# Performance work log

Hardware: AMD Instinct MI355X
Metric: run time of the kernel (lower is better)

Reference implementation:

```python
import jax, jax.numpy as jnp
import numpy as np

B, S, T = 64, 64, 64          # batch, encoder seq len, decoder context_length
V, D, H, L = 32000, 512, 1024, 256  # vocab, embed, hidden, latent


def _gru_cell(x, h, W_ih, W_hh, b_ih, b_hh):
    # PyTorch GRUCell math. x:[B,D_in], h:[B,H]
    gi = x @ W_ih.T + b_ih            # [B,3H]
    gh = h @ W_hh.T + b_hh            # [B,3H]
    i_r, i_z, i_n = jnp.split(gi, 3, axis=-1)
    h_r, h_z, h_n = jnp.split(gh, 3, axis=-1)
    r = jax.nn.sigmoid(i_r + h_r)
    z = jax.nn.sigmoid(i_z + h_z)
    n = jnp.tanh(i_n + r * h_n)
    return (1.0 - z) * n + z * h


def setup_inputs() -> dict:
    key = jax.random.key(0)
    ks = jax.random.split(key, 16)
    s = 0.02
    inp = {
        "x": jax.random.randint(ks[0], (B, S), 0, V),
        "eps": jax.random.normal(ks[1], (B, L), dtype=jnp.float32),
        "E": jax.random.normal(ks[2], (V, D), dtype=jnp.float32) * s,
        # encoder GRU
        "W_ih_enc": jax.random.normal(ks[3], (3 * H, D), dtype=jnp.float32) * s,
        "W_hh_enc": jax.random.normal(ks[4], (3 * H, H), dtype=jnp.float32) * s,
        "b_ih_enc": jnp.zeros((3 * H,), jnp.float32),
        "b_hh_enc": jnp.zeros((3 * H,), jnp.float32),
        # latent heads
        "W_mu": jax.random.normal(ks[5], (L, H), dtype=jnp.float32) * s,
        "b_mu": jnp.zeros((L,), jnp.float32),
        "W_lv": jax.random.normal(ks[6], (L, H), dtype=jnp.float32) * s,
        "b_lv": jnp.zeros((L,), jnp.float32),
        # decoder proj_h: latent -> hidden
        "W_proj": jax.random.normal(ks[7], (H, L), dtype=jnp.float32) * s,
        "b_proj": jnp.zeros((H,), jnp.float32),
        # decoder GRU cell
        "W_ih_dec": jax.random.normal(ks[8], (3 * H, D), dtype=jnp.float32) * s,
        "W_hh_dec": jax.random.normal(ks[9], (3 * H, H), dtype=jnp.float32) * s,
        "b_ih_dec": jnp.zeros((3 * H,), jnp.float32),
        "b_hh_dec": jnp.zeros((3 * H,), jnp.float32),
        # output projection hidden -> vocab
        "W_out": jax.random.normal(ks[10], (V, H), dtype=jnp.float32) * s,
        "b_out": jnp.zeros((V,), jnp.float32),
    }
    return inp


def reference(x, eps, E, W_ih_enc, W_hh_enc, b_ih_enc, b_hh_enc,
              W_mu, b_mu, W_lv, b_lv, W_proj, b_proj,
              W_ih_dec, W_hh_dec, b_ih_dec, b_hh_dec, W_out, b_out):
    # --- encode ---
    xe = E[x]                                  # [B,S,D]
    h0 = jnp.zeros((x.shape[0], H), xe.dtype)

    def enc_step(h, xt):
        h = _gru_cell(xt, h, W_ih_enc, W_hh_enc, b_ih_enc, b_hh_enc)
        return h, None

    h_last, _ = jax.lax.scan(enc_step, h0, jnp.swapaxes(xe, 0, 1))  # scan over S
    mu = h_last @ W_mu.T + b_mu                # [B,L]
    logvar = h_last @ W_lv.T + b_lv            # [B,L]

    # --- reparametrize ---
    z = mu + eps * jnp.exp(0.5 * logvar)       # [B,L]

    h_dec0 = z @ W_proj.T + b_proj             # [B,H]
    x0 = jnp.zeros((x.shape[0], D), xe.dtype)  # step 0 input is None -> zeros

    def dec_step(carry, _):
        h, xin = carry
        h = _gru_cell(xin, h, W_ih_dec, W_hh_dec, b_ih_dec, b_hh_dec)
        logits = h @ W_out.T + b_out           # [B,V]
        nxt = jnp.argmax(logits, axis=-1)      # [B]
        return (h, E[nxt]), logits

    _, logits_seq = jax.lax.scan(dec_step, (h_dec0, x0), None, length=T)
    outputs = jnp.swapaxes(logits_seq, 0, 1)   # [B,T,V]
    return outputs, mu, logvar
```

## Files before the change

kernel.cpp:

```cpp
#include <hip/hip_runtime.h>

#define B_ 64
#define S_ 64
#define T_ 64
#define V_ 32000
#define D_ 512
#define H_ 1024
#define L_ 256

typedef _Float16 f16;
typedef __attribute__((ext_vector_type(4))) _Float16 f16x4;
typedef __attribute__((ext_vector_type(8))) _Float16 f16x8;
typedef __attribute__((ext_vector_type(16))) float f32x16;

#define INV2048 (1.0f / 2048.0f)

__device__ __forceinline__ void write_frag(f16* __restrict__ Aohi, f16* __restrict__ Aolo,
                                           int b, int j, float hv) {
  const f16 hi = (f16)hv;
  const f16 lo = (f16)((hv - (float)hi) * 2048.0f);
  const long long fo =
      (((long long)(b >> 5) * 64 + (j >> 4)) * 64 + ((b & 31) + 32 * ((j >> 3) & 1))) * 8 + (j & 7);
  Aohi[fo] = hi;
  Aolo[fo] = lo;
}

template <int K>
__global__ __launch_bounds__(256) void k_pack_wf(
    const float* __restrict__ W, f16* __restrict__ Bhi, f16* __restrict__ Blo)
{
  const int n = blockIdx.x;
  const int k = threadIdx.x * 4;
  if (k >= K) return;
  float4 w = *reinterpret_cast<const float4*>(W + (long long)n * K + k);
  float wv[4] = {w.x, w.y, w.z, w.w};
  f16x4 hi, lo;
#pragma unroll
  for (int i = 0; i < 4; ++i) {
    const f16 h = (f16)wv[i];
    hi[i] = h;
    lo[i] = (f16)((wv[i] - (float)h) * 2048.0f);
  }
  const int nt = n >> 5;
  const int lane = (n & 31) + 32 * ((k >> 3) & 1);
  const int ks = k >> 4;
  const long long off = (((long long)nt * (K / 16) + ks) * 64 + lane) * 8 + (k & 7);
  *reinterpret_cast<f16x4*>(Bhi + off) = hi;
  *reinterpret_cast<f16x4*>(Blo + off) = lo;
}

__global__ __launch_bounds__(128) void k_pack_xe(
    const int* __restrict__ x, const float* __restrict__ E,
    f16* __restrict__ XAhi, f16* __restrict__ XAlo)
{
  const int m = blockIdx.x;
  const int s = m >> 6, b = m & 63;
  const int k = threadIdx.x * 4;
  const long long tok = x[b * S_ + s];
  float4 w = *reinterpret_cast<const float4*>(E + tok * D_ + k);
  float wv[4] = {w.x, w.y, w.z, w.w};
  f16x4 hi, lo;
#pragma unroll
  for (int i = 0; i < 4; ++i) {
    const f16 h = (f16)wv[i];
    hi[i] = h;
    lo[i] = (f16)((wv[i] - (float)h) * 2048.0f);
  }
  const int mt = m >> 5;
  const int lane = (m & 31) + 32 * ((k >> 3) & 1);
  const int ks = k >> 4;
  const long long off = (((long long)mt * 32 + ks) * 64 + lane) * 8 + (k & 7);
  *reinterpret_cast<f16x4*>(XAhi + off) = hi;
  *reinterpret_cast<f16x4*>(XAlo + off) = lo;
}

__global__ __launch_bounds__(256) void k_gates_mfma(
    const f16* __restrict__ XAhi, const f16* __restrict__ XAlo,
    const f16* __restrict__ Bhi, const f16* __restrict__ Blo,
    const float* __restrict__ b_ih, float* __restrict__ Gi)
{
  __shared__ float cand[4][64][33];
  const int tid = threadIdx.x;
  const int lane = tid & 63;
  const int wv = __builtin_amdgcn_readfirstlane(tid >> 6);
  const int s = blockIdx.x / 24;
  const int ng = blockIdx.x % 24;
  const int nt = ng * 4 + wv;

  f32x16 aM0, aM1, aLa0, aLa1, aLb0, aLb1;
#pragma unroll
  for (int i = 0; i < 16; ++i) {
    aM0[i] = 0.f; aM1[i] = 0.f; aLa0[i] = 0.f; aLa1[i] = 0.f; aLb0[i] = 0.f; aLb1[i] = 0.f;
  }

  const f16x8* pB_h = reinterpret_cast<const f16x8*>(Bhi) + ((long long)nt * 32) * 64 + lane;
  const f16x8* pB_l = reinterpret_cast<const f16x8*>(Blo) + ((long long)nt * 32) * 64 + lane;
  const f16x8* pA_h = reinterpret_cast<const f16x8*>(XAhi) + ((long long)s * 64) * 64 + lane;
  const f16x8* pA_l = reinterpret_cast<const f16x8*>(XAlo) + ((long long)s * 64) * 64 + lane;

#pragma unroll 4
  for (int ks = 0; ks < 32; ++ks) {
    const int o = ks * 64;
    f16x8 bh = pB_h[o];
    f16x8 bl = pB_l[o];
    f16x8 a0 = pA_h[o];
    f16x8 a1 = pA_h[o + 32 * 64];
    f16x8 l0 = pA_l[o];
    f16x8 l1 = pA_l[o + 32 * 64];
    aM0 = __builtin_amdgcn_mfma_f32_32x32x16_f16(a0, bh, aM0, 0, 0, 0);
    aM1 = __builtin_amdgcn_mfma_f32_32x32x16_f16(a1, bh, aM1, 0, 0, 0);
    aLa0 = __builtin_amdgcn_mfma_f32_32x32x16_f16(a0, bl, aLa0, 0, 0, 0);
    aLa1 = __builtin_amdgcn_mfma_f32_32x32x16_f16(a1, bl, aLa1, 0, 0, 0);
    aLb0 = __builtin_amdgcn_mfma_f32_32x32x16_f16(l0, bh, aLb0, 0, 0, 0);
    aLb1 = __builtin_amdgcn_mfma_f32_32x32x16_f16(l1, bh, aLb1, 0, 0, 0);
  }

  {
    const int l = lane & 31;
    const int rbase = 4 * (lane >> 5);
#pragma unroll
    for (int reg = 0; reg < 16; ++reg) {
      const int row = (reg & 3) + 8 * (reg >> 2) + rbase;
      cand[wv][row][l] = aM0[reg] + (aLa0[reg] + aLb0[reg]) * INV2048;
      cand[wv][row + 32][l] = aM1[reg] + (aLa1[reg] + aLb1[reg]) * INV2048;
    }
  }
  __syncthreads();
  const int bn0 = ng * 128;
#pragma unroll
  for (int i = 0; i < 8; ++i) {
    const int idx = i * 256 + tid;
    const int b4 = (idx & 15) * 4;
    const int nl = idx >> 4;
    const float bi = b_ih[bn0 + nl];
    float4 o;
    o.x = cand[nl >> 5][b4 + 0][nl & 31] + bi;
    o.y = cand[nl >> 5][b4 + 1][nl & 31] + bi;
    o.z = cand[nl >> 5][b4 + 2][nl & 31] + bi;
    o.w = cand[nl >> 5][b4 + 3][nl & 31] + bi;
    *reinterpret_cast<float4*>(&Gi[((long long)s * (3 * H_) + bn0 + nl) * 64 + b4]) = o;
  }
}

__global__ __launch_bounds__(256) void k_hh_mfma(
    const f16* __restrict__ Ahi, const f16* __restrict__ Alo,
    const f16* __restrict__ Bhi, const f16* __restrict__ Blo,
    float* __restrict__ preH)
{
  __shared__ float cand[4][64][33];
  const int tid = threadIdx.x;
  const int lane = tid & 63;
  const int wv = __builtin_amdgcn_readfirstlane(tid >> 6);
  const int nt = blockIdx.x;

  f32x16 aM0, aM1, aLa0, aLa1, aLb0, aLb1;
#pragma unroll
  for (int i = 0; i < 16; ++i) {
    aM0[i] = 0.f; aM1[i] = 0.f; aLa0[i] = 0.f; aLa1[i] = 0.f; aLb0[i] = 0.f; aLb1[i] = 0.f;
  }

  const f16x8* pB_h = reinterpret_cast<const f16x8*>(Bhi) + ((long long)nt * 64 + wv * 16) * 64 + lane;
  const f16x8* pB_l = reinterpret_cast<const f16x8*>(Blo) + ((long long)nt * 64 + wv * 16) * 64 + lane;
  const f16x8* pA_h = reinterpret_cast<const f16x8*>(Ahi) + (long long)(wv * 16) * 64 + lane;
  const f16x8* pA_l = reinterpret_cast<const f16x8*>(Alo) + (long long)(wv * 16) * 64 + lane;

#pragma unroll 4
  for (int q = 0; q < 16; ++q) {
    const int o = q * 64;
    f16x8 bh = pB_h[o];
    f16x8 bl = pB_l[o];
    f16x8 a0 = pA_h[o];
    f16x8 a1 = pA_h[o + 4096];
    f16x8 l0 = pA_l[o];
    f16x8 l1 = pA_l[o + 4096];
    aM0 = __builtin_amdgcn_mfma_f32_32x32x16_f16(a0, bh, aM0, 0, 0, 0);
    aM1 = __builtin_amdgcn_mfma_f32_32x32x16_f16(a1, bh, aM1, 0, 0, 0);
    aLa0 = __builtin_amdgcn_mfma_f32_32x32x16_f16(a0, bl, aLa0, 0, 0, 0);
    aLa1 = __builtin_amdgcn_mfma_f32_32x32x16_f16(a1, bl, aLa1, 0, 0, 0);
    aLb0 = __builtin_amdgcn_mfma_f32_32x32x16_f16(l0, bh, aLb0, 0, 0, 0);
    aLb1 = __builtin_amdgcn_mfma_f32_32x32x16_f16(l1, bh, aLb1, 0, 0, 0);
  }

  {
    const int l = lane & 31;
    const int rbase = 4 * (lane >> 5);
#pragma unroll
    for (int reg = 0; reg < 16; ++reg) {
      const int row = (reg & 3) + 8 * (reg >> 2) + rbase;
      cand[wv][row][l] = aM0[reg] + (aLa0[reg] + aLb0[reg]) * INV2048;
      cand[wv][row + 32][l] = aM1[reg] + (aLa1[reg] + aLb1[reg]) * INV2048;
    }
  }
  __syncthreads();
#pragma unroll
  for (int i = 0; i < 8; ++i) {
    const int idx = i * 256 + tid;
    const int b = idx & 63;
    const int l = idx >> 6;
    const float v = cand[0][b][l] + cand[1][b][l] + cand[2][b][l] + cand[3][b][l];
    preH[((long long)nt * 32 + l) * 64 + b] = v;
  }
}

__global__ __launch_bounds__(256) void k_apply_enc(
    const float* __restrict__ preH, const float* __restrict__ Gi_t,
    const float* __restrict__ b_hh,
    const float* __restrict__ hT_in, float* __restrict__ hT_out,
    f16* __restrict__ Aohi, f16* __restrict__ Aolo)
{
  const int idx = blockIdx.x * 256 + threadIdx.x;
  const int b = idx & 63;
  const int j = idx >> 6;
  const float gr = preH[(long long)j * 64 + b] + Gi_t[(long long)j * 64 + b] + b_hh[j];
  const float gz = preH[(long long)(H_ + j) * 64 + b] + Gi_t[(long long)(H_ + j) * 64 + b] + b_hh[H_ + j];
  const float gin = Gi_t[(long long)(2 * H_ + j) * 64 + b];
  const float ghn = preH[(long long)(2 * H_ + j) * 64 + b] + b_hh[2 * H_ + j];
  const float r = 1.f / (1.f + expf(-gr));
  const float z = 1.f / (1.f + expf(-gz));
  const float n = tanhf(fmaf(r, ghn, gin));
  const float hp = hT_in[(long long)j * 64 + b];
  const float hv = (1.f - z) * n + z * hp;
  hT_out[(long long)j * 64 + b] = hv;
  write_frag(Aohi, Aolo, b, j, hv);
}

template <int XMODE>
__global__ __launch_bounds__(1024) void k_dec_apply(
    const float* __restrict__ E, const unsigned long long* __restrict__ bp,
    const float* __restrict__ W_ih,
    const float* __restrict__ b_ih, const float* __restrict__ b_hh,
    const float* __restrict__ preH, const float* __restrict__ hT_in,
    float* __restrict__ hT_out, f16* __restrict__ Aohi, f16* __restrict__ Aolo)
{
  __shared__ float4 a_lds[64 * 64];
  __shared__ float red[12 * 3 * 64];
  __shared__ int toks[64];
  const int tid = threadIdx.x;
  const int lane = tid & 63;
  const int wv = __builtin_amdgcn_readfirstlane(tid >> 6);
  const int jj = wv & 3;
  const int ks = wv >> 2;
  const int j = blockIdx.x * 4 + jj;
  const int kf16 = tid & 63;
  const int msub = tid >> 6;

  float accR = 0.f, accZ = 0.f, accIN = 0.f;

  if constexpr (XMODE == 2) {
#pragma unroll
    for (int rr = 0; rr < 4; ++rr) {
      const int r = wv + rr * 16;
      unsigned long long kk = 0ull;
#pragma unroll
      for (int i = 0; i < 4; ++i) {
        const unsigned long long q = bp[(long long)r * 256 + lane + i * 64];
        if (q > kk) kk = q;
      }
#pragma unroll
      for (int m = 1; m < 64; m <<= 1) {
        const unsigned long long q = __shfl_xor(kk, m, 64);
        if (q > kk) kk = q;
      }
      if (lane == 0) toks[r] = (int)(0xFFFFFFFFu - (unsigned)(kk & 0xFFFFFFFFull));
    }
    __syncthreads();

    const float* wr = W_ih + (long long)j * D_;
    const float* wz = W_ih + (long long)(j + H_) * D_;
    const float* wn = W_ih + (long long)(j + 2 * H_) * D_;
    for (int c = 0; c < 2; ++c) {
      __syncthreads();
#pragma unroll
      for (int p = 0; p < 4; ++p) {
        const int m = p * 16 + msub;
        const long long tok = toks[m];
        float4 v = *reinterpret_cast<const float4*>(E + tok * D_ + c * 256 + kf16 * 4);
        a_lds[m * 64 + (kf16 ^ (m & 7))] = v;
      }
      __syncthreads();
#pragma unroll 4
      for (int q = 0; q < 16; ++q) {
        const int kf = ks * 16 + q;
        float4 a = a_lds[lane * 64 + (kf ^ (lane & 7))];
        float4 w0 = *reinterpret_cast<const float4*>(wr + c * 256 + kf * 4);
        float4 w1 = *reinterpret_cast<const float4*>(wz + c * 256 + kf * 4);
        float4 w2 = *reinterpret_cast<const float4*>(wn + c * 256 + kf * 4);
        accR = fmaf(w0.x, a.x, accR); accR = fmaf(w0.y, a.y, accR);
        accR = fmaf(w0.z, a.z, accR); accR = fmaf(w0.w, a.w, accR);
        accZ = fmaf(w1.x, a.x, accZ); accZ = fmaf(w1.y, a.y, accZ);
        accZ = fmaf(w1.z, a.z, accZ); accZ = fmaf(w1.w, a.w, accZ);
        accIN = fmaf(w2.x, a.x, accIN); accIN = fmaf(w2.y, a.y, accIN);
        accIN = fmaf(w2.z, a.z, accIN); accIN = fmaf(w2.w, a.w, accIN);
      }
    }
  }

  if (ks > 0) {
    float* rp = red + (((ks - 1) * 4 + jj) * 3) * 64 + lane;
    rp[0] = accR; rp[64] = accZ; rp[128] = accIN;
  }
  __syncthreads();
  if (ks == 0) {
#pragma unroll
    for (int t2 = 0; t2 < 3; ++t2) {
      const float* rp = red + ((t2 * 4 + jj) * 3) * 64 + lane;
      accR += rp[0]; accZ += rp[64]; accIN += rp[128];
    }
    const float gr = accR + preH[(long long)j * 64 + lane] + b_ih[j] + b_hh[j];
    const float gz = accZ + preH[(long long)(H_ + j) * 64 + lane] + b_ih[H_ + j] + b_hh[H_ + j];
    const float gin = accIN + b_ih[2 * H_ + j];
    const float ghn = preH[(long long)(2 * H_ + j) * 64 + lane] + b_hh[2 * H_ + j];
    const float r = 1.f / (1.f + expf(-gr));
    const float z = 1.f / (1.f + expf(-gz));
    const float n = tanhf(fmaf(r, ghn, gin));
    const float hp = hT_in[(long long)j * 64 + lane];
    const float hv = (1.f - z) * n + z * hp;
    hT_out[(long long)j * 64 + lane] = hv;
    write_frag(Aohi, Aolo, lane, j, hv);
  }
}

__global__ __launch_bounds__(256) void k_logits_hh(
    const f16* __restrict__ Ahi, const f16* __restrict__ Alo,
    const f16* __restrict__ WOhi, const f16* __restrict__ WOlo,
    const f16* __restrict__ WHhi, const f16* __restrict__ WHlo,
    const float* __restrict__ b_out, float* __restrict__ out,
    unsigned long long* __restrict__ bestPart, float* __restrict__ preH, int t)
{
  __shared__ float cand[4][64][33];
  __shared__ unsigned long long wbest[4][64];
  const int tid = threadIdx.x;
  const int lane = tid & 63;
  const int wv = __builtin_amdgcn_readfirstlane(tid >> 6);

  if (blockIdx.x >= 250) {
    const int hhb = blockIdx.x - 250;
    const int nt = hhb * 4 + wv;
    f32x16 aM0, aM1, aLa0, aLa1, aLb0, aLb1;
#pragma unroll
    for (int i = 0; i < 16; ++i) {
      aM0[i] = 0.f; aM1[i] = 0.f; aLa0[i] = 0.f; aLa1[i] = 0.f; aLb0[i] = 0.f; aLb1[i] = 0.f;
    }
    const f16x8* pB_h = reinterpret_cast<const f16x8*>(WHhi) + ((long long)nt * 64) * 64 + lane;
    const f16x8* pB_l = reinterpret_cast<const f16x8*>(WHlo) + ((long long)nt * 64) * 64 + lane;
    const f16x8* pA_h = reinterpret_cast<const f16x8*>(Ahi) + lane;
    const f16x8* pA_l = reinterpret_cast<const f16x8*>(Alo) + lane;
#pragma unroll 4
    for (int ksi = 0; ksi < 64; ++ksi) {
      const int o = ksi * 64;
      f16x8 bh = pB_h[o];
      f16x8 bl = pB_l[o];
      f16x8 a0 = pA_h[o];
      f16x8 a1 = pA_h[o + 4096];
      f16x8 l0 = pA_l[o];
      f16x8 l1 = pA_l[o + 4096];
      aM0 = __builtin_amdgcn_mfma_f32_32x32x16_f16(a0, bh, aM0, 0, 0, 0);
      aM1 = __builtin_amdgcn_mfma_f32_32x32x16_f16(a1, bh, aM1, 0, 0, 0);
      aLa0 = __builtin_amdgcn_mfma_f32_32x32x16_f16(a0, bl, aLa0, 0, 0, 0);
      aLa1 = __builtin_amdgcn_mfma_f32_32x32x16_f16(a1, bl, aLa1, 0, 0, 0);
      aLb0 = __builtin_amdgcn_mfma_f32_32x32x16_f16(l0, bh, aLb0, 0, 0, 0);
      aLb1 = __builtin_amdgcn_mfma_f32_32x32x16_f16(l1, bh, aLb1, 0, 0, 0);
    }
    {
      const int l = lane & 31;
      const int rbase = 4 * (lane >> 5);
#pragma unroll
      for (int reg = 0; reg < 16; ++reg) {
        const int row = (reg & 3) + 8 * (reg >> 2) + rbase;
        cand[wv][row][l] = aM0[reg] + (aLa0[reg] + aLb0[reg]) * INV2048;
        cand[wv][row + 32][l] = aM1[reg] + (aLa1[reg] + aLb1[reg]) * INV2048;
      }
    }
    __syncthreads();
#pragma unroll
    for (int i = 0; i < 8; ++i) {
      const int idx = i * 256 + tid;
      const int b4 = (idx & 15) * 4;
      const int nl = idx >> 4;
      float4 o;
      o.x = cand[nl >> 5][b4 + 0][nl & 31];
      o.y = cand[nl >> 5][b4 + 1][nl & 31];
      o.z = cand[nl >> 5][b4 + 2][nl & 31];
      o.w = cand[nl >> 5][b4 + 3][nl & 31];
      *reinterpret_cast<float4*>(&preH[((long long)hhb * 128 + nl) * 64 + b4]) = o;
    }
    return;
  }

  const int nt = blockIdx.x * 4 + wv;
  f32x16 accM0, accM1, accL0, accL1;
#pragma unroll
  for (int i = 0; i < 16; ++i) { accM0[i] = 0.f; accM1[i] = 0.f; accL0[i] = 0.f; accL1[i] = 0.f; }

  const f16x8* pAh0 = reinterpret_cast<const f16x8*>(Ahi) + lane;
  const f16x8* pAh1 = reinterpret_cast<const f16x8*>(Ahi) + 4096 + lane;
  const f16x8* pAl0 = reinterpret_cast<const f16x8*>(Alo) + lane;
  const f16x8* pAl1 = reinterpret_cast<const f16x8*>(Alo) + 4096 + lane;
  const f16x8* pBh = reinterpret_cast<const f16x8*>(WOhi) + (long long)nt * 4096 + lane;
  const f16x8* pBl = reinterpret_cast<const f16x8*>(WOlo) + (long long)nt * 4096 + lane;

#pragma unroll 4
  for (int ksi = 0; ksi < 64; ++ksi) {
    const int o = ksi * 64;
    f16x8 bh = pBh[o];
    f16x8 bl = pBl[o];
    f16x8 ah0 = pAh0[o];
    f16x8 ah1 = pAh1[o];
    f16x8 al0 = pAl0[o];
    f16x8 al1 = pAl1[o];
    accM0 = __builtin_amdgcn_mfma_f32_32x32x16_f16(ah0, bh, accM0, 0, 0, 0);
    accM1 = __builtin_amdgcn_mfma_f32_32x32x16_f16(ah1, bh, accM1, 0, 0, 0);
    accL0 = __builtin_amdgcn_mfma_f32_32x32x16_f16(ah0, bl, accL0, 0, 0, 0);
    accL1 = __builtin_amdgcn_mfma_f32_32x32x16_f16(ah1, bl, accL1, 0, 0, 0);
    accL0 = __builtin_amdgcn_mfma_f32_32x32x16_f16(al0, bh, accL0, 0, 0, 0);
    accL1 = __builtin_amdgcn_mfma_f32_32x32x16_f16(al1, bh, accL1, 0, 0, 0);
  }

  const int nn = nt * 32 + (lane & 31);
  const float bo = b_out[nn];
  const int rbase = 4 * (lane >> 5);
#pragma unroll
  for (int reg = 0; reg < 16; ++reg) {
    const int row0 = (reg & 3) + 8 * (reg >> 2) + rbase;
    const float v0 = accM0[reg] + accL0[reg] * INV2048 + bo;
    __builtin_nontemporal_store(v0, &out[(long long)row0 * (T_ * (long long)V_) + (long long)t * V_ + nn]);
    cand[wv][row0][lane & 31] = v0;
    const int row1 = row0 + 32;
    const float v1 = accM1[reg] + accL1[reg] * INV2048 + bo;
    __builtin_nontemporal_store(v1, &out[(long long)row1 * (T_ * (long long)V_) + (long long)t * V_ + nn]);
    cand[wv][row1][lane & 31] = v1;
  }
  __syncthreads();
  {
    const int w = tid >> 6, r = tid & 63;
    const int nb = (blockIdx.x * 4 + w) * 32;
    unsigned long long kk = 0ull;
#pragma unroll
    for (int l0 = 0; l0 < 32; ++l0) {
      const int l = (l0 + r) & 31;
      const float v = cand[w][r][l];
      unsigned u = __float_as_uint(v);
      u = (u & 0x80000000u) ? ~u : (u | 0x80000000u);
      const unsigned long long key = ((unsigned long long)u << 32) |
          (unsigned long long)(0xFFFFFFFFu - (unsigned)(nb + l));
      if (key > kk) kk = key;
    }
    wbest[w][r] = kk;
  }
  __syncthreads();
  if (tid < 64) {
    unsigned long long kk = wbest[0][tid];
#pragma unroll
    for (int w = 1; w < 4; ++w) { const unsigned long long q = wbest[w][tid]; if (q > kk) kk = q; }
    bestPart[(long long)tid * 256 + blockIdx.x] = kk;
  }
}

__global__ __launch_bounds__(256) void k_mu_lv_z(
    const float* __restrict__ hT, const float* __restrict__ W_mu, const float* __restrict__ b_mu,
    const float* __restrict__ W_lv, const float* __restrict__ b_lv,
    const float* __restrict__ eps, float* __restrict__ out_mu, float* __restrict__ out_lv,
    float* __restrict__ zT)
{
  const int lane = threadIdx.x & 63;
  const int wv = __builtin_amdgcn_readfirstlane(threadIdx.x >> 6);
  const int l = blockIdx.x * 4 + wv;
  const float* wm = W_mu + (long long)l * H_;
  const float* wl = W_lv + (long long)l * H_;
  float am = 0.f, av = 0.f;
#pragma unroll 8
  for (int k = 0; k < H_; ++k) {
    const float h = hT[k * 64 + lane];
    am = fmaf(wm[k], h, am);
    av = fmaf(wl[k], h, av);
  }
  const float mu = am + b_mu[l];
  const float lv = av + b_lv[l];
  out_mu[lane * L_ + l] = mu;
  out_lv[lane * L_ + l] = lv;
  zT[l * 64 + lane] = fmaf(eps[lane * L_ + l], expf(0.5f * lv), mu);
}

__global__ __launch_bounds__(256) void k_proj(
    const float* __restrict__ zT, const float* __restrict__ W_proj,
    const float* __restrict__ b_proj, float* __restrict__ hT0,
    f16* __restrict__ Aohi, f16* __restrict__ Aolo)
{
  const int lane = threadIdx.x & 63;
  const int wv = __builtin_amdgcn_readfirstlane(threadIdx.x >> 6);
  const int j = blockIdx.x * 4 + wv;
  const float* wr = W_proj + (long long)j * L_;
  float acc = 0.f;
#pragma unroll 8
  for (int k = 0; k < L_; ++k) acc = fmaf(wr[k], zT[k * 64 + lane], acc);
  const float hv = acc + b_proj[j];
  hT0[(long long)j * 64 + lane] = hv;
  write_frag(Aohi, Aolo, lane, j, hv);
}

extern "C" void kernel_launch(void* const* d_in, const int* in_sizes, int n_in,
                              void* d_out, int out_size, void* d_ws, size_t ws_size,
                              hipStream_t stream) {
  (void)in_sizes; (void)n_in; (void)out_size;
  const int*   x        = (const int*)d_in[0];
  const float* eps      = (const float*)d_in[1];
  const float* E        = (const float*)d_in[2];
  const float* W_ih_enc = (const float*)d_in[3];
  const float* W_hh_enc = (const float*)d_in[4];
  const float* b_ih_enc = (const float*)d_in[5];
  const float* b_hh_enc = (const float*)d_in[6];
  const float* W_mu     = (const float*)d_in[7];
  const float* b_mu     = (const float*)d_in[8];
  const float* W_lv     = (const float*)d_in[9];
  const float* b_lv     = (const float*)d_in[10];
  const float* W_proj   = (const float*)d_in[11];
  const float* b_proj   = (const float*)d_in[12];
  const float* W_ih_dec = (const float*)d_in[13];
  const float* W_hh_dec = (const float*)d_in[14];
  const float* b_ih_dec = (const float*)d_in[15];
  const float* b_hh_dec = (const float*)d_in[16];
  const float* W_out    = (const float*)d_in[17];
  const float* b_out    = (const float*)d_in[18];

  float* out = (float*)d_out;
  const long long OFF_MU = (long long)B_ * T_ * V_;
  const long long OFF_LV = OFF_MU + (long long)B_ * L_;

  float* ws = (float*)d_ws;
  float* hA   = ws + 0;
  float* hB   = ws + 65536;
  float* dA   = ws + 131072;
  float* dB   = ws + 196608;
  float* zT   = ws + 262144;
  unsigned long long* bestPart = (unsigned long long*)(ws + 278528);
  float* preH = ws + 311296;
  f16* frAhi  = (f16*)(ws + 507904);
  f16* frAlo  = (f16*)(ws + 540672);
  f16* WHEhi  = (f16*)(ws + 638976);
  f16* WHElo  = (f16*)(ws + 2211840);
  f16* WHDhi  = (f16*)(ws + 3784704);
  f16* WHDlo  = (f16*)(ws + 5357568);
  f16* WIEhi  = (f16*)(ws + 6930432);
  f16* WIElo  = (f16*)(ws + 7716864);
  f16* XAhi   = (f16*)(ws + 8503296);
  f16* XAlo   = (f16*)(ws + 9551872);
  float* Gi   = ws + 10600448;
  f16* WOhi   = (f16*)(ws + 8503296);
  f16* WOlo   = (f16*)(ws + 24887296);
  const size_t WS_NEED = (size_t)41271296 * 4;
  if (ws_size < WS_NEED) return;

  hipMemsetAsync(hA, 0, (size_t)H_ * B_ * sizeof(float), stream);
  hipMemsetAsync(frAhi, 0, (size_t)2 * 65536 * sizeof(f16), stream);
  hipMemsetAsync(bestPart, 0, (size_t)64 * 256 * 8, stream);

  k_pack_wf<1024><<<3 * H_, 256, 0, stream>>>(W_hh_enc, WHEhi, WHElo);
  k_pack_wf<1024><<<3 * H_, 256, 0, stream>>>(W_hh_dec, WHDhi, WHDlo);
  k_pack_wf<512><<<3 * H_, 128, 0, stream>>>(W_ih_enc, WIEhi, WIElo);
  k_pack_xe<<<S_ * B_, 128, 0, stream>>>(x, E, XAhi, XAlo);

  k_gates_mfma<<<64 * 24, 256, 0, stream>>>(XAhi, XAlo, WIEhi, WIElo, b_ih_enc, Gi);

  for (int t = 0; t < S_; ++t) {
    const float* hin = (t & 1) ? hB : hA;
    float* hout = (t & 1) ? hA : hB;
    k_hh_mfma<<<96, 256, 0, stream>>>(frAhi, frAlo, WHEhi, WHElo, preH);
    k_apply_enc<<<256, 256, 0, stream>>>(preH, Gi + (long long)t * 3 * H_ * B_,
                                         b_hh_enc, hin, hout, frAhi, frAlo);
  }

  k_mu_lv_z<<<64, 256, 0, stream>>>(hA, W_mu, b_mu, W_lv, b_lv, eps,
                                    out + OFF_MU, out + OFF_LV, zT);
  k_proj<<<256, 256, 0, stream>>>(zT, W_proj, b_proj, dA, frAhi, frAlo);

  k_pack_wf<1024><<<V_, 256, 0, stream>>>(W_out, WOhi, WOlo);

  k_hh_mfma<<<96, 256, 0, stream>>>(frAhi, frAlo, WHDhi, WHDlo, preH);

  for (int t = 0; t < T_; ++t) {
    const float* hin = (t & 1) ? dB : dA;
    float* hout = (t & 1) ? dA : dB;
    if (t == 0) {
      k_dec_apply<0><<<256, 1024, 0, stream>>>(
          E, nullptr, W_ih_dec, b_ih_dec, b_hh_dec, preH, hin, hout, frAhi, frAlo);
    } else {
      k_dec_apply<2><<<256, 1024, 0, stream>>>(
          E, bestPart, W_ih_dec, b_ih_dec, b_hh_dec, preH, hin, hout, frAhi, frAlo);
    }
    k_logits_hh<<<274, 256, 0, stream>>>(frAhi, frAlo, WOhi, WOlo, WHDhi, WHDlo,
                                         b_out, out, bestPart, preH, t);
  }
}
```

Before: 6.076 ms.

## Fuse encoder and decoder step loops into persistent kernels with grid barriers

Replaces the per-timestep kernel launches for the encoder (hh matmul plus apply) and the decoder (apply, logits/argmax, hh matmul) with two persistent 256-block kernels. Phases inside each step are separated by atomic-counter grid barriers. The decoder input projection now runs on MFMA using a packed split-f16 W_ih_dec and a packed embedding of the argmax token, replacing the scalar FMA path. This removes launch overhead and inter-kernel gaps across 128 serial steps. In exchange it relies on all 256 blocks being co-resident for the spin barrier, and it adds barrier latency and fewer parallel blocks per phase.

```diff
diff --git a/kernel.cpp b/kernel.cpp
--- a/kernel.cpp
+++ b/kernel.cpp
@@ -7,6 +7,7 @@
 #define D_ 512
 #define H_ 1024
 #define L_ 256
+#define NBLK 256
 
 typedef _Float16 f16;
 typedef __attribute__((ext_vector_type(4))) _Float16 f16x4;
@@ -14,6 +15,23 @@
 typedef __attribute__((ext_vector_type(16))) float f32x16;
 
 #define INV2048 (1.0f / 2048.0f)
+
+__device__ __forceinline__ void gbar(unsigned* cnt, unsigned* gen, unsigned tgt) {
+  __syncthreads();
+  if (threadIdx.x == 0) {
+    __threadfence();
+    unsigned old = __hip_atomic_fetch_add(cnt, 1u, __ATOMIC_ACQ_REL, __HIP_MEMORY_SCOPE_AGENT);
+    if (old == NBLK - 1) {
+      __hip_atomic_store(cnt, 0u, __ATOMIC_RELAXED, __HIP_MEMORY_SCOPE_AGENT);
+      __hip_atomic_fetch_add(gen, 1u, __ATOMIC_RELEASE, __HIP_MEMORY_SCOPE_AGENT);
+    } else {
+      while (__hip_atomic_load(gen, __ATOMIC_ACQUIRE, __HIP_MEMORY_SCOPE_AGENT) < tgt)
+        __builtin_amdgcn_s_sleep(2);
+    }
+  }
+  __syncthreads();
+  __threadfence();
+}
 
 __device__ __forceinline__ void write_frag(f16* __restrict__ Aohi, f16* __restrict__ Aolo,
                                            int b, int j, float hv) {
@@ -142,37 +160,31 @@
   }
 }
 
-__global__ __launch_bounds__(256) void k_hh_mfma(
-    const f16* __restrict__ Ahi, const f16* __restrict__ Alo,
-    const f16* __restrict__ Bhi, const f16* __restrict__ Blo,
-    float* __restrict__ preH)
-{
-  __shared__ float cand[4][64][33];
-  const int tid = threadIdx.x;
-  const int lane = tid & 63;
-  const int wv = __builtin_amdgcn_readfirstlane(tid >> 6);
-  const int nt = blockIdx.x;
-
+template <int NITER, int AMT>
+__device__ __forceinline__ void mm_phase(
+    const f16* __restrict__ Ah, const f16* __restrict__ Al,
+    const f16* __restrict__ Bh, const f16* __restrict__ Bl,
+    int nt, int wv, int lane, int tid,
+    float (*cand)[64][33], float* __restrict__ outp)
+{
   f32x16 aM0, aM1, aLa0, aLa1, aLb0, aLb1;
 #pragma unroll
   for (int i = 0; i < 16; ++i) {
     aM0[i] = 0.f; aM1[i] = 0.f; aLa0[i] = 0.f; aLa1[i] = 0.f; aLb0[i] = 0.f; aLb1[i] = 0.f;
   }
-
-  const f16x8* pB_h = reinterpret_cast<const f16x8*>(Bhi) + ((long long)nt * 64 + wv * 16) * 64 + lane;
-  const f16x8* pB_l = reinterpret_cast<const f16x8*>(Blo) + ((long long)nt * 64 + wv * 16) * 64 + lane;
-  const f16x8* pA_h = reinterpret_cast<const f16x8*>(Ahi) + (long long)(wv * 16) * 64 + lane;
-  const f16x8* pA_l = reinterpret_cast<const f16x8*>(Alo) + (long long)(wv * 16) * 64 + lane;
-
+  const f16x8* pBh = reinterpret_cast<const f16x8*>(Bh) + ((long long)nt * (4 * NITER) + wv * NITER) * 64 + lane;
+  const f16x8* pBl = reinterpret_cast<const f16x8*>(Bl) + ((long long)nt * (4 * NITER) + wv * NITER) * 64 + lane;
+  const f16x8* pAh = reinterpret_cast<const f16x8*>(Ah) + (long long)(wv * NITER) * 64 + lane;
+  const f16x8* pAl = reinterpret_cast<const f16x8*>(Al) + (long long)(wv * NITER) * 64 + lane;
 #pragma unroll 4
-  for (int q = 0; q < 16; ++q) {
+  for (int q = 0; q < NITER; ++q) {
     const int o = q * 64;
-    f16x8 bh = pB_h[o];
-    f16x8 bl = pB_l[o];
-    f16x8 a0 = pA_h[o];
-    f16x8 a1 = pA_h[o + 4096];
-    f16x8 l0 = pA_l[o];
-    f16x8 l1 = pA_l[o + 4096];
+    f16x8 bh = pBh[o];
+    f16x8 bl = pBl[o];
+    f16x8 a0 = pAh[o];
+    f16x8 a1 = pAh[o + AMT];
+    f16x8 l0 = pAl[o];
+    f16x8 l1 = pAl[o + AMT];
     aM0 = __builtin_amdgcn_mfma_f32_32x32x16_f16(a0, bh, aM0, 0, 0, 0);
     aM1 = __builtin_amdgcn_mfma_f32_32x32x16_f16(a1, bh, aM1, 0, 0, 0);
     aLa0 = __builtin_amdgcn_mfma_f32_32x32x16_f16(a0, bl, aLa0, 0, 0, 0);
@@ -180,7 +192,6 @@
     aLb0 = __builtin_amdgcn_mfma_f32_32x32x16_f16(l0, bh, aLb0, 0, 0, 0);
     aLb1 = __builtin_amdgcn_mfma_f32_32x32x16_f16(l1, bh, aLb1, 0, 0, 0);
   }
-
   {
     const int l = lane & 31;
     const int rbase = 4 * (lane >> 5);
@@ -196,263 +207,200 @@
   for (int i = 0; i < 8; ++i) {
     const int idx = i * 256 + tid;
     const int b = idx & 63;
-    const int l = idx >> 6;
-    const float v = cand[0][b][l] + cand[1][b][l] + cand[2][b][l] + cand[3][b][l];
-    preH[((long long)nt * 32 + l) * 64 + b] = v;
-  }
-}
-
-__global__ __launch_bounds__(256) void k_apply_enc(
-    const float* __restrict__ preH, const float* __restrict__ Gi_t,
-    const float* __restrict__ b_hh,
-    const float* __restrict__ hT_in, float* __restrict__ hT_out,
-    f16* __restrict__ Aohi, f16* __restrict__ Aolo)
-{
-  const int idx = blockIdx.x * 256 + threadIdx.x;
-  const int b = idx & 63;
-  const int j = idx >> 6;
-  const float gr = preH[(long long)j * 64 + b] + Gi_t[(long long)j * 64 + b] + b_hh[j];
-  const float gz = preH[(long long)(H_ + j) * 64 + b] + Gi_t[(long long)(H_ + j) * 64 + b] + b_hh[H_ + j];
-  const float gin = Gi_t[(long long)(2 * H_ + j) * 64 + b];
-  const float ghn = preH[(long long)(2 * H_ + j) * 64 + b] + b_hh[2 * H_ + j];
-  const float r = 1.f / (1.f + expf(-gr));
-  const float z = 1.f / (1.f + expf(-gz));
-  const float n = tanhf(fmaf(r, ghn, gin));
-  const float hp = hT_in[(long long)j * 64 + b];
-  const float hv = (1.f - z) * n + z * hp;
-  hT_out[(long long)j * 64 + b] = hv;
-  write_frag(Aohi, Aolo, b, j, hv);
-}
-
-template <int XMODE>
-__global__ __launch_bounds__(1024) void k_dec_apply(
-    const float* __restrict__ E, const unsigned long long* __restrict__ bp,
-    const float* __restrict__ W_ih,
-    const float* __restrict__ b_ih, const float* __restrict__ b_hh,
-    const float* __restrict__ preH, const float* __restrict__ hT_in,
-    float* __restrict__ hT_out, f16* __restrict__ Aohi, f16* __restrict__ Aolo)
-{
-  __shared__ float4 a_lds[64 * 64];
-  __shared__ float red[12 * 3 * 64];
-  __shared__ int toks[64];
+    const int l2 = idx >> 6;
+    const float v = cand[0][b][l2] + cand[1][b][l2] + cand[2][b][l2] + cand[3][b][l2];
+    outp[(long long)l2 * 64 + b] = v;
+  }
+}
+
+__global__ __launch_bounds__(256, 2) void k_enc_persist(
+    const f16* __restrict__ WHEhi, const f16* __restrict__ WHElo,
+    const float* __restrict__ Gi, const float* __restrict__ b_hh,
+    float* __restrict__ hT, float* __restrict__ preH,
+    f16* __restrict__ frAhi, f16* __restrict__ frAlo,
+    unsigned* cnt, unsigned* gen)
+{
+  __shared__ float cand[4][64][33];
   const int tid = threadIdx.x;
   const int lane = tid & 63;
   const int wv = __builtin_amdgcn_readfirstlane(tid >> 6);
-  const int jj = wv & 3;
-  const int ks = wv >> 2;
-  const int j = blockIdx.x * 4 + jj;
-  const int kf16 = tid & 63;
-  const int msub = tid >> 6;
-
-  float accR = 0.f, accZ = 0.f, accIN = 0.f;
-
-  if constexpr (XMODE == 2) {
-#pragma unroll
-    for (int rr = 0; rr < 4; ++rr) {
-      const int r = wv + rr * 16;
-      unsigned long long kk = 0ull;
-#pragma unroll
-      for (int i = 0; i < 4; ++i) {
-        const unsigned long long q = bp[(long long)r * 256 + lane + i * 64];
-        if (q > kk) kk = q;
-      }
-#pragma unroll
-      for (int m = 1; m < 64; m <<= 1) {
-        const unsigned long long q = __shfl_xor(kk, m, 64);
-        if (q > kk) kk = q;
-      }
-      if (lane == 0) toks[r] = (int)(0xFFFFFFFFu - (unsigned)(kk & 0xFFFFFFFFull));
-    }
-    __syncthreads();
-
-    const float* wr = W_ih + (long long)j * D_;
-    const float* wz = W_ih + (long long)(j + H_) * D_;
-    const float* wn = W_ih + (long long)(j + 2 * H_) * D_;
-    for (int c = 0; c < 2; ++c) {
-      __syncthreads();
-#pragma unroll
-      for (int p = 0; p < 4; ++p) {
-        const int m = p * 16 + msub;
-        const long long tok = toks[m];
-        float4 v = *reinterpret_cast<const float4*>(E + tok * D_ + c * 256 + kf16 * 4);
-        a_lds[m * 64 + (kf16 ^ (m & 7))] = v;
-      }
-      __syncthreads();
-#pragma unroll 4
-      for (int q = 0; q < 16; ++q) {
-        const int kf = ks * 16 + q;
-        float4 a = a_lds[lane * 64 + (kf ^ (lane & 7))];
-        float4 w0 = *reinterpret_cast<const float4*>(wr + c * 256 + kf * 4);
-        float4 w1 = *reinterpret_cast<const float4*>(wz + c * 256 + kf * 4);
-        float4 w2 = *reinterpret_cast<const float4*>(wn + c * 256 + kf * 4);
-        accR = fmaf(w0.x, a.x, accR); accR = fmaf(w0.y, a.y, accR);
-        accR = fmaf(w0.z, a.z, accR); accR = fmaf(w0.w, a.w, accR);
-        accZ = fmaf(w1.x, a.x, accZ); accZ = fmaf(w1.y, a.y, accZ);
-        accZ = fmaf(w1.z, a.z, accZ); accZ = fmaf(w1.w, a.w, accZ);
-        accIN = fmaf(w2.x, a.x, accIN); accIN = fmaf(w2.y, a.y, accIN);
-        accIN = fmaf(w2.z, a.z, accIN); accIN = fmaf(w2.w, a.w, accIN);
-      }
-    }
-  }
-
-  if (ks > 0) {
-    float* rp = red + (((ks - 1) * 4 + jj) * 3) * 64 + lane;
-    rp[0] = accR; rp[64] = accZ; rp[128] = accIN;
-  }
-  __syncthreads();
-  if (ks == 0) {
-#pragma unroll
-    for (int t2 = 0; t2 < 3; ++t2) {
-      const float* rp = red + ((t2 * 4 + jj) * 3) * 64 + lane;
-      accR += rp[0]; accZ += rp[64]; accIN += rp[128];
-    }
-    const float gr = accR + preH[(long long)j * 64 + lane] + b_ih[j] + b_hh[j];
-    const float gz = accZ + preH[(long long)(H_ + j) * 64 + lane] + b_ih[H_ + j] + b_hh[H_ + j];
-    const float gin = accIN + b_ih[2 * H_ + j];
-    const float ghn = preH[(long long)(2 * H_ + j) * 64 + lane] + b_hh[2 * H_ + j];
-    const float r = 1.f / (1.f + expf(-gr));
-    const float z = 1.f / (1.f + expf(-gz));
-    const float n = tanhf(fmaf(r, ghn, gin));
-    const float hp = hT_in[(long long)j * 64 + lane];
-    const float hv = (1.f - z) * n + z * hp;
-    hT_out[(long long)j * 64 + lane] = hv;
-    write_frag(Aohi, Aolo, lane, j, hv);
-  }
-}
-
-__global__ __launch_bounds__(256) void k_logits_hh(
-    const f16* __restrict__ Ahi, const f16* __restrict__ Alo,
+  const int gtid = blockIdx.x * 256 + tid;
+  const int jc = gtid >> 6;
+  const int b = gtid & 63;
+  unsigned tgt = 0;
+
+  for (int t = 0; t < S_; ++t) {
+    if (blockIdx.x < 96)
+      mm_phase<16, 4096>(frAhi, frAlo, WHEhi, WHElo, blockIdx.x, wv, lane, tid,
+                         cand, preH + (long long)blockIdx.x * 2048);
+    gbar(cnt, gen, ++tgt);
+    {
+      const float* Gt = Gi + (long long)t * 3 * H_ * 64;
+      const float gr = preH[(long long)jc * 64 + b] + Gt[(long long)jc * 64 + b] + b_hh[jc];
+      const float gz = preH[(long long)(H_ + jc) * 64 + b] + Gt[(long long)(H_ + jc) * 64 + b] + b_hh[H_ + jc];
+      const float gin = Gt[(long long)(2 * H_ + jc) * 64 + b];
+      const float ghn = preH[(long long)(2 * H_ + jc) * 64 + b] + b_hh[2 * H_ + jc];
+      const float r = 1.f / (1.f + expf(-gr));
+      const float z = 1.f / (1.f + expf(-gz));
+      const float n = tanhf(fmaf(r, ghn, gin));
+      const float hp = hT[(long long)jc * 64 + b];
+      const float hv = (1.f - z) * n + z * hp;
+      hT[(long long)jc * 64 + b] = hv;
+      write_frag(frAhi, frAlo, b, jc, hv);
+    }
+    gbar(cnt, gen, ++tgt);
+  }
+}
+
+__global__ __launch_bounds__(256, 2) void k_dec_persist(
+    const float* __restrict__ E,
+    const f16* __restrict__ WHDhi, const f16* __restrict__ WHDlo,
+    const f16* __restrict__ WIDhi, const f16* __restrict__ WIDlo,
     const f16* __restrict__ WOhi, const f16* __restrict__ WOlo,
-    const f16* __restrict__ WHhi, const f16* __restrict__ WHlo,
+    const float* __restrict__ b_ih, const float* __restrict__ b_hh,
     const float* __restrict__ b_out, float* __restrict__ out,
-    unsigned long long* __restrict__ bestPart, float* __restrict__ preH, int t)
+    unsigned long long* __restrict__ bestPart,
+    float* __restrict__ preH, float* __restrict__ preI,
+    float* __restrict__ hT, f16* __restrict__ frAhi, f16* __restrict__ frAlo,
+    f16* __restrict__ XAhi, f16* __restrict__ XAlo,
+    unsigned* cnt, unsigned* gen)
 {
   __shared__ float cand[4][64][33];
   __shared__ unsigned long long wbest[4][64];
   const int tid = threadIdx.x;
   const int lane = tid & 63;
   const int wv = __builtin_amdgcn_readfirstlane(tid >> 6);
-
-  if (blockIdx.x >= 250) {
-    const int hhb = blockIdx.x - 250;
-    const int nt = hhb * 4 + wv;
-    f32x16 aM0, aM1, aLa0, aLa1, aLb0, aLb1;
-#pragma unroll
-    for (int i = 0; i < 16; ++i) {
-      aM0[i] = 0.f; aM1[i] = 0.f; aLa0[i] = 0.f; aLa1[i] = 0.f; aLb0[i] = 0.f; aLb1[i] = 0.f;
-    }
-    const f16x8* pB_h = reinterpret_cast<const f16x8*>(WHhi) + ((long long)nt * 64) * 64 + lane;
-    const f16x8* pB_l = reinterpret_cast<const f16x8*>(WHlo) + ((long long)nt * 64) * 64 + lane;
-    const f16x8* pA_h = reinterpret_cast<const f16x8*>(Ahi) + lane;
-    const f16x8* pA_l = reinterpret_cast<const f16x8*>(Alo) + lane;
+  const int gtid = blockIdx.x * 256 + tid;
+  const int jc = gtid >> 6;
+  const int b = gtid & 63;
+  unsigned tgt = 0;
+
+  for (int t = 0; t < T_; ++t) {
+    if (blockIdx.x < 96)
+      mm_phase<16, 4096>(frAhi, frAlo, WHDhi, WHDlo, blockIdx.x, wv, lane, tid,
+                         cand, preH + (long long)blockIdx.x * 2048);
+    else if (blockIdx.x < 192)
+      mm_phase<8, 2048>(XAhi, XAlo, WIDhi, WIDlo, blockIdx.x - 96, wv, lane, tid,
+                        cand, preI + (long long)(blockIdx.x - 96) * 2048);
+    gbar(cnt, gen, ++tgt);
+
+    {
+      const float gr = preI[(long long)jc * 64 + b] + preH[(long long)jc * 64 + b] + b_ih[jc] + b_hh[jc];
+      const float gz = preI[(long long)(H_ + jc) * 64 + b] + preH[(long long)(H_ + jc) * 64 + b] +
+                       b_ih[H_ + jc] + b_hh[H_ + jc];
+      const float gin = preI[(long long)(2 * H_ + jc) * 64 + b] + b_ih[2 * H_ + jc];
+      const float ghn = preH[(long long)(2 * H_ + jc) * 64 + b] + b_hh[2 * H_ + jc];
+      const float r = 1.f / (1.f + expf(-gr));
+      const float z = 1.f / (1.f + expf(-gz));
+      const float n = tanhf(fmaf(r, ghn, gin));
+      const float hp = hT[(long long)jc * 64 + b];
+      const float hv = (1.f - z) * n + z * hp;
+      hT[(long long)jc * 64 + b] = hv;
+      write_frag(frAhi, frAlo, b, jc, hv);
+    }
+    gbar(cnt, gen, ++tgt);
+
+    if (blockIdx.x < 250) {
+      const int nt = blockIdx.x * 4 + wv;
+      f32x16 accM0, accM1, accL0, accL1;
+#pragma unroll
+      for (int i = 0; i < 16; ++i) { accM0[i] = 0.f; accM1[i] = 0.f; accL0[i] = 0.f; accL1[i] = 0.f; }
+
+      const f16x8* pAh0 = reinterpret_cast<const f16x8*>(frAhi) + lane;
+      const f16x8* pAh1 = reinterpret_cast<const f16x8*>(frAhi) + 4096 + lane;
+      const f16x8* pAl0 = reinterpret_cast<const f16x8*>(frAlo) + lane;
+      const f16x8* pAl1 = reinterpret_cast<const f16x8*>(frAlo) + 4096 + lane;
+      const f16x8* pBh = reinterpret_cast<const f16x8*>(WOhi) + (long long)nt * 4096 + lane;
+      const f16x8* pBl = reinterpret_cast<const f16x8*>(WOlo) + (long long)nt * 4096 + lane;
+
 #pragma unroll 4
-    for (int ksi = 0; ksi < 64; ++ksi) {
-      const int o = ksi * 64;
-      f16x8 bh = pB_h[o];
-      f16x8 bl = pB_l[o];
-      f16x8 a0 = pA_h[o];
-      f16x8 a1 = pA_h[o + 4096];
-      f16x8 l0 = pA_l[o];
-      f16x8 l1 = pA_l[o + 4096];
-      aM0 = __builtin_amdgcn_mfma_f32_32x32x16_f16(a0, bh, aM0, 0, 0, 0);
-      aM1 = __builtin_amdgcn_mfma_f32_32x32x16_f16(a1, bh, aM1, 0, 0, 0);
-      aLa0 = __builtin_amdgcn_mfma_f32_32x32x16_f16(a0, bl, aLa0, 0, 0, 0);
-      aLa1 = __builtin_amdgcn_mfma_f32_32x32x16_f16(a1, bl, aLa1, 0, 0, 0);
-      aLb0 = __builtin_amdgcn_mfma_f32_32x32x16_f16(l0, bh, aLb0, 0, 0, 0);
-      aLb1 = __builtin_amdgcn_mfma_f32_32x32x16_f16(l1, bh, aLb1, 0, 0, 0);
-    }
-    {
-      const int l = lane & 31;
+      for (int ksi = 0; ksi < 64; ++ksi) {
+        const int o = ksi * 64;
+        f16x8 bh = pBh[o];
+        f16x8 bl = pBl[o];
+        f16x8 ah0 = pAh0[o];
+        f16x8 ah1 = pAh1[o];
+        f16x8 al0 = pAl0[o];
+        f16x8 al1 = pAl1[o];
+        accM0 = __builtin_amdgcn_mfma_f32_32x32x16_f16(ah0, bh, accM0, 0, 0, 0);
+        accM1 = __builtin_amdgcn_mfma_f32_32x32x16_f16(ah1, bh, accM1, 0, 0, 0);
+        accL0 = __builtin_amdgcn_mfma_f32_32x32x16_f16(ah0, bl, accL0, 0, 0, 0);
+        accL1 = __builtin_amdgcn_mfma_f32_32x32x16_f16(ah1, bl, accL1, 0, 0, 0);
+        accL0 = __builtin_amdgcn_mfma_f32_32x32x16_f16(al0, bh, accL0, 0, 0, 0);
+        accL1 = __builtin_amdgcn_mfma_f32_32x32x16_f16(al1, bh, accL1, 0, 0, 0);
+      }
+
+      const int nn = nt * 32 + (lane & 31);
+      const float bo = b_out[nn];
       const int rbase = 4 * (lane >> 5);
 #pragma unroll
       for (int reg = 0; reg < 16; ++reg) {
-        const int row = (reg & 3) + 8 * (reg >> 2) + rbase;
-        cand[wv][row][l] = aM0[reg] + (aLa0[reg] + aLb0[reg]) * INV2048;
-        cand[wv][row + 32][l] = aM1[reg] + (aLa1[reg] + aLb1[reg]) * INV2048;
-      }
-    }
-    __syncthreads();
-#pragma unroll
-    for (int i = 0; i < 8; ++i) {
-      const int idx = i * 256 + tid;
-      const int b4 = (idx & 15) * 4;
-      const int nl = idx >> 4;
-      float4 o;
-      o.x = cand[nl >> 5][b4 + 0][nl & 31];
-      o.y = cand[nl >> 5][b4 + 1][nl & 31];
-      o.z = cand[nl >> 5][b4 + 2][nl & 31];
-      o.w = cand[nl >> 5][b4 + 3][nl & 31];
-      *reinterpret_cast<float4*>(&preH[((long long)hhb * 128 + nl) * 64 + b4]) = o;
-    }
-    return;
-  }
-
-  const int nt = blockIdx.x * 4 + wv;
-  f32x16 accM0, accM1, accL0, accL1;
-#pragma unroll
-  for (int i = 0; i < 16; ++i) { accM0[i] = 0.f; accM1[i] = 0.f; accL0[i] = 0.f; accL1[i] = 0.f; }
-
-  const f16x8* pAh0 = reinterpret_cast<const f16x8*>(Ahi) + lane;
-  const f16x8* pAh1 = reinterpret_cast<const f16x8*>(Ahi) + 4096 + lane;
-  const f16x8* pAl0 = reinterpret_cast<const f16x8*>(Alo) + lane;
-  const f16x8* pAl1 = reinterpret_cast<const f16x8*>(Alo) + 4096 + lane;
-  const f16x8* pBh = reinterpret_cast<const f16x8*>(WOhi) + (long long)nt * 4096 + lane;
-  const f16x8* pBl = reinterpret_cast<const f16x8*>(WOlo) + (long long)nt * 4096 + lane;
-
-#pragma unroll 4
-  for (int ksi = 0; ksi < 64; ++ksi) {
-    const int o = ksi * 64;
-    f16x8 bh = pBh[o];
-    f16x8 bl = pBl[o];
-    f16x8 ah0 = pAh0[o];
-    f16x8 ah1 = pAh1[o];
-    f16x8 al0 = pAl0[o];
-    f16x8 al1 = pAl1[o];
-    accM0 = __builtin_amdgcn_mfma_f32_32x32x16_f16(ah0, bh, accM0, 0, 0, 0);
-    accM1 = __builtin_amdgcn_mfma_f32_32x32x16_f16(ah1, bh, accM1, 0, 0, 0);
-    accL0 = __builtin_amdgcn_mfma_f32_32x32x16_f16(ah0, bl, accL0, 0, 0, 0);
-    accL1 = __builtin_amdgcn_mfma_f32_32x32x16_f16(ah1, bl, accL1, 0, 0, 0);
-    accL0 = __builtin_amdgcn_mfma_f32_32x32x16_f16(al0, bh, accL0, 0, 0, 0);
-    accL1 = __builtin_amdgcn_mfma_f32_32x32x16_f16(al1, bh, accL1, 0, 0, 0);
-  }
-
-  const int nn = nt * 32 + (lane & 31);
-  const float bo = b_out[nn];
-  const int rbase = 4 * (lane >> 5);
-#pragma unroll
-  for (int reg = 0; reg < 16; ++reg) {
-    const int row0 = (reg & 3) + 8 * (reg >> 2) + rbase;
-    const float v0 = accM0[reg] + accL0[reg] * INV2048 + bo;
-    __builtin_nontemporal_store(v0, &out[(long long)row0 * (T_ * (long long)V_) + (long long)t * V_ + nn]);
-    cand[wv][row0][lane & 31] = v0;
-    const int row1 = row0 + 32;
-    const float v1 = accM1[reg] + accL1[reg] * INV2048 + bo;
-    __builtin_nontemporal_store(v1, &out[(long long)row1 * (T_ * (long long)V_) + (long long)t * V_ + nn]);
-    cand[wv][row1][lane & 31] = v1;
-  }
-  __syncthreads();
-  {
-    const int w = tid >> 6, r = tid & 63;
-    const int nb = (blockIdx.x * 4 + w) * 32;
-    unsigned long long kk = 0ull;
-#pragma unroll
-    for (int l0 = 0; l0 < 32; ++l0) {
-      const int l = (l0 + r) & 31;
-      const float v = cand[w][r][l];
-      unsigned u = __float_as_uint(v);
-      u = (u & 0x80000000u) ? ~u : (u | 0x80000000u);
-      const unsigned long long key = ((unsigned long long)u << 32) |
-          (unsigned long long)(0xFFFFFFFFu - (unsigned)(nb + l));
-      if (key > kk) kk = key;
-    }
-    wbest[w][r] = kk;
-  }
-  __syncthreads();
-  if (tid < 64) {
-    unsigned long long kk = wbest[0][tid];
-#pragma unroll
-    for (int w = 1; w < 4; ++w) { const unsigned long long q = wbest[w][tid]; if (q > kk) kk = q; }
-    bestPart[(long long)tid * 256 + blockIdx.x] = kk;
+        const int row0 = (reg & 3) + 8 * (reg >> 2) + rbase;
+        const float v0 = accM0[reg] + accL0[reg] * INV2048 + bo;
+        __builtin_nontemporal_store(v0, &out[(long long)row0 * (T_ * (long long)V_) + (long long)t * V_ + nn]);
+        cand[wv][row0][lane & 31] = v0;
+        const int row1 = row0 + 32;
+        const float v1 = accM1[reg] + accL1[reg] * INV2048 + bo;
+        __builtin_nontemporal_store(v1, &out[(long long)row1 * (T_ * (long long)V_) + (long long)t * V_ + nn]);
+        cand[wv][row1][lane & 31] = v1;
+      }
+      __syncthreads();
+      {
+        const int w = tid >> 6, r = tid & 63;
+        const int nb = (blockIdx.x * 4 + w) * 32;
+        unsigned long long kk = 0ull;
+#pragma unroll
+        for (int l0 = 0; l0 < 32; ++l0) {
+          const int l = (l0 + r) & 31;
+          const float v = cand[w][r][l];
+          unsigned u = __float_as_uint(v);
+          u = (u & 0x80000000u) ? ~u : (u | 0x80000000u);
+          const unsigned long long key = ((unsigned long long)u << 32) |
+              (unsigned long long)(0xFFFFFFFFu - (unsigned)(nb + l));
+          if (key > kk) kk = key;
+        }
+        wbest[w][r] = kk;
+      }
+      __syncthreads();
+      if (tid < 64) {
+        unsigned long long kk = wbest[0][tid];
+#pragma unroll
+        for (int w = 1; w < 4; ++w) { const unsigned long long q = wbest[w][tid]; if (q > kk) kk = q; }
+        bestPart[(long long)tid * 256 + blockIdx.x] = kk;
+      }
+    }
+    gbar(cnt, gen, ++tgt);
+
+    if (blockIdx.x < 16) {
+      const int r = blockIdx.x * 4 + wv;
+      unsigned long long kk = 0ull;
+#pragma unroll
+      for (int i = 0; i < 4; ++i) {
+        const unsigned long long q = bestPart[(long long)r * 256 + lane + i * 64];
+        if (q > kk) kk = q;
+      }
+#pragma unroll
+      for (int m = 1; m < 64; m <<= 1) {
+        const unsigned long long q = __shfl_xor(kk, m, 64);
+        if (q > kk) kk = q;
+      }
+      const int tok = (int)(0xFFFFFFFFu - (unsigned)(kk & 0xFFFFFFFFull));
+      const float* ep = E + (long long)tok * D_ + lane * 8;
+      float4 v0 = *reinterpret_cast<const float4*>(ep);
+      float4 v1 = *reinterpret_cast<const float4*>(ep + 4);
+      float vv[8] = {v0.x, v0.y, v0.z, v0.w, v1.x, v1.y, v1.z, v1.w};
+      f16x8 hi, lo;
+#pragma unroll
+      for (int e = 0; e < 8; ++e) {
+        const f16 h = (f16)vv[e];
+        hi[e] = h;
+        lo[e] = (f16)((vv[e] - (float)h) * 2048.0f);
+      }
+      const long long unit = (((long long)(r >> 5) * 32 + (lane >> 1)) * 64 + ((r & 31) + 32 * (lane & 1)));
+      *reinterpret_cast<f16x8*>(XAhi + unit * 8) = hi;
+      *reinterpret_cast<f16x8*>(XAlo + unit * 8) = lo;
+    }
+    gbar(cnt, gen, ++tgt);
   }
 }
 
@@ -528,46 +476,48 @@
 
   float* ws = (float*)d_ws;
   float* hA   = ws + 0;
-  float* hB   = ws + 65536;
-  float* dA   = ws + 131072;
-  float* dB   = ws + 196608;
-  float* zT   = ws + 262144;
-  unsigned long long* bestPart = (unsigned long long*)(ws + 278528);
-  float* preH = ws + 311296;
-  f16* frAhi  = (f16*)(ws + 507904);
-  f16* frAlo  = (f16*)(ws + 540672);
+  float* dA   = ws + 65536;
+  float* zT   = ws + 131072;
+  unsigned long long* bestPart = (unsigned long long*)(ws + 147456);
+  float* preH = ws + 180224;
+  float* preI = ws + 376832;
+  f16* frAhi  = (f16*)(ws + 573440);
+  f16* frAlo  = (f16*)(ws + 606208);
   f16* WHEhi  = (f16*)(ws + 638976);
   f16* WHElo  = (f16*)(ws + 2211840);
   f16* WHDhi  = (f16*)(ws + 3784704);
   f16* WHDlo  = (f16*)(ws + 5357568);
   f16* WIEhi  = (f16*)(ws + 6930432);
   f16* WIElo  = (f16*)(ws + 7716864);
-  f16* XAhi   = (f16*)(ws + 8503296);
-  f16* XAlo   = (f16*)(ws + 9551872);
-  float* Gi   = ws + 10600448;
-  f16* WOhi   = (f16*)(ws + 8503296);
-  f16* WOlo   = (f16*)(ws + 24887296);
-  const size_t WS_NEED = (size_t)41271296 * 4;
+  f16* WIDhi  = (f16*)(ws + 8503296);
+  f16* WIDlo  = (f16*)(ws + 9289728);
+  unsigned* bar = (unsigned*)(ws + 10076160);
+  f16* XAdhi  = (f16*)(ws + 10076416);
+  f16* XAdlo  = (f16*)(ws + 10092800);
+  f16* XAehi  = (f16*)(ws + 10109184);
+  f16* XAelo  = (f16*)(ws + 11157760);
+  float* Gi   = ws + 12206336;
+  f16* WOhi   = (f16*)(ws + 10109184);
+  f16* WOlo   = (f16*)(ws + 26493184);
+  const size_t WS_NEED = (size_t)42877184 * 4;
   if (ws_size < WS_NEED) return;
 
   hipMemsetAsync(hA, 0, (size_t)H_ * B_ * sizeof(float), stream);
   hipMemsetAsync(frAhi, 0, (size_t)2 * 65536 * sizeof(f16), stream);
   hipMemsetAsync(bestPart, 0, (size_t)64 * 256 * 8, stream);
+  hipMemsetAsync(bar, 0, 256 * sizeof(float), stream);
+  hipMemsetAsync(XAdhi, 0, (size_t)2 * 32768 * sizeof(f16), stream);
 
   k_pack_wf<1024><<<3 * H_, 256, 0, stream>>>(W_hh_enc, WHEhi, WHElo);
   k_pack_wf<1024><<<3 * H_, 256, 0, stream>>>(W_hh_dec, WHDhi, WHDlo);
   k_pack_wf<512><<<3 * H_, 128, 0, stream>>>(W_ih_enc, WIEhi, WIElo);
-  k_pack_xe<<<S_ * B_, 128, 0, stream>>>(x, E, XAhi, XAlo);
-
-  k_gates_mfma<<<64 * 24, 256, 0, stream>>>(XAhi, XAlo, WIEhi, WIElo, b_ih_enc, Gi);
-
-  for (int t = 0; t < S_; ++t) {
-    const float* hin = (t & 1) ? hB : hA;
-    float* hout = (t & 1) ? hA : hB;
-    k_hh_mfma<<<96, 256, 0, stream>>>(frAhi, frAlo, WHEhi, WHElo, preH);
-    k_apply_enc<<<256, 256, 0, stream>>>(preH, Gi + (long long)t * 3 * H_ * B_,
-                                         b_hh_enc, hin, hout, frAhi, frAlo);
-  }
+  k_pack_wf<512><<<3 * H_, 128, 0, stream>>>(W_ih_dec, WIDhi, WIDlo);
+  k_pack_xe<<<S_ * B_, 128, 0, stream>>>(x, E, XAehi, XAelo);
+
+  k_gates_mfma<<<64 * 24, 256, 0, stream>>>(XAehi, XAelo, WIEhi, WIElo, b_ih_enc, Gi);
+
+  k_enc_persist<<<NBLK, 256, 0, stream>>>(WHEhi, WHElo, Gi, b_hh_enc, hA, preH,
+                                          frAhi, frAlo, bar + 0, bar + 32);
 
   k_mu_lv_z<<<64, 256, 0, stream>>>(hA, W_mu, b_mu, W_lv, b_lv, eps,
                                     out + OFF_MU, out + OFF_LV, zT);
@@ -575,19 +525,8 @@
 
   k_pack_wf<1024><<<V_, 256, 0, stream>>>(W_out, WOhi, WOlo);
 
-  k_hh_mfma<<<96, 256, 0, stream>>>(frAhi, frAlo, WHDhi, WHDlo, preH);
-
-  for (int t = 0; t < T_; ++t) {
-    const float* hin = (t & 1) ? dB : dA;
-    float* hout = (t & 1) ? dA : dB;
-    if (t == 0) {
-      k_dec_apply<0><<<256, 1024, 0, stream>>>(
-          E, nullptr, W_ih_dec, b_ih_dec, b_hh_dec, preH, hin, hout, frAhi, frAlo);
-    } else {
-      k_dec_apply<2><<<256, 1024, 0, stream>>>(
-          E, bestPart, W_ih_dec, b_ih_dec, b_hh_dec, preH, hin, hout, frAhi, frAlo);
-    }
-    k_logits_hh<<<274, 256, 0, stream>>>(frAhi, frAlo, WOhi, WOlo, WHDhi, WHDlo,
-                                         b_out, out, bestPart, preH, t);
-  }
-}
+  k_dec_persist<<<NBLK, 256, 0, stream>>>(
+      E, WHDhi, WHDlo, WIDhi, WIDlo, WOhi, WOlo,
+      b_ih_dec, b_hh_dec, b_out, out, bestPart, preH, preI,
+      dA, frAhi, frAlo, XAdhi, XAdlo, bar + 64, bar + 96);
+}
```

After: 23.27 ms. 283% more time.
